# Optimization experiments

Hardware: AMD Instinct MI355X
Metric: run time of the kernel (lower is better)

Reference implementation:

```python
import jax, jax.numpy as jnp
import numpy as np

N = 50000      # nodes
E = 800000     # edges (before self-loops)
IN = 256       # input features
H = 8          # heads
C = 32         # hidden channels per head
OUT = 40       # classes
NEG_SLOPE = 0.2


def setup_inputs() -> dict:
    key = jax.random.key(0)
    ks = jax.random.split(key, 12)
    sd = lambda k, sh: (jax.random.normal(k, sh, jnp.float32) * 0.05)
    return {
        "x": jax.random.normal(ks[0], (N, IN), jnp.float32),
        "edge_index": jax.random.randint(ks[1], (2, E), 0, N),
        "W1": sd(ks[2], (IN, H * C)),
        "a_src1": sd(ks[3], (H, C)),
        "a_dst1": sd(ks[4], (H, C)),
        "b1": jnp.zeros((C,), jnp.float32),
        "W2": sd(ks[5], (C, H * C)),
        "a_src2": sd(ks[6], (H, C)),
        "a_dst2": sd(ks[7], (H, C)),
        "b2": jnp.zeros((C,), jnp.float32),
        "Wo": sd(ks[8], (C, OUT)),
        "bo": jnp.zeros((OUT,), jnp.float32),
    }


def gat_layer(x, src, dst, n, W, a_src, a_dst, b):
    # x: [N, F]; src/dst: [E'] (self-loops included). concat=False -> mean over heads.
    h = (x @ W).reshape(n, H, C)                       # [N, H, C]
    alpha_src = jnp.sum(h * a_src, axis=-1)            # [N, H]
    alpha_dst = jnp.sum(h * a_dst, axis=-1)            # [N, H]
    e = alpha_src[src] + alpha_dst[dst]                # [E', H]
    e = jnp.where(e > 0, e, NEG_SLOPE * e)             # leaky_relu
    # segment softmax over incoming edges of each dst node
    m = jax.ops.segment_max(e, dst, num_segments=n)    # [N, H]
    ex = jnp.exp(e - m[dst])                           # [E', H]
    s = jax.ops.segment_sum(ex, dst, num_segments=n)   # [N, H]
    alpha = ex / s[dst]                                # [E', H]
    msg = alpha[:, :, None] * h[src]                   # [E', H, C]
    out = jax.ops.segment_sum(msg, dst, num_segments=n)  # [N, H, C]
    return out.mean(axis=1) + b                        # [N, C]


def reference(x, edge_index, W1, a_src1, a_dst1, b1, W2, a_src2, a_dst2, b2, Wo, bo):
    n = x.shape[0]
    loops = jnp.arange(n, dtype=edge_index.dtype)
    src = jnp.concatenate([edge_index[0], loops])      # add self-loops (PyG default)
    dst = jnp.concatenate([edge_index[1], loops])
    h = gat_layer(x, src, dst, n, W1, a_src1, a_dst1, b1)
    h = jax.nn.elu(h)                                  # dropout skipped (eval)
    h = gat_layer(h, src, dst, n, W2, a_src2, a_dst2, b2)
    h = jax.nn.elu(h)
    logits = h @ Wo + bo
    return jax.nn.log_softmax(logits, axis=1)
```

## Files before the change

kernel.cpp:

```cpp
#include <hip/hip_runtime.h>
#include <math.h>

#define N_NODES 50000
#define N_PAD   50016
#define N_EDGES 800000
#define E_TOT   (N_EDGES + N_NODES)
#define F_IN    256
#define NHEAD   8
#define CH      32
#define HC      256
#define OUT_C   40
#define NEG_SLOPE 0.2f
#define SCAN_BLOCKS ((N_NODES + 255) / 256)
#define G_WCVT  ((HC * F_IN + 255) / 256)
#define G_WCVT2 ((HC * CH + 255) / 256)
#define NRANGE  8
#define RANGE_SZ (N_NODES / NRANGE)
#define BIN_CHUNK 2048
#define G_BINCH ((E_TOT + BIN_CHUNK - 1) / BIN_CHUNK)

typedef unsigned short u16;
typedef unsigned int   u32;
typedef unsigned char  u8;
typedef __attribute__((ext_vector_type(8))) short bf16x8;
typedef __attribute__((ext_vector_type(4))) float f32x4;
typedef __attribute__((ext_vector_type(2))) float f32x2;

__device__ __forceinline__ u16 f2bf(float f) {
    union { u32 u; float f; } x; x.f = f;
    u32 u = x.u;
    return (u16)((u + 0x7fffu + ((u >> 16) & 1u)) >> 16);
}
__device__ __forceinline__ float bflo(u32 v) {
    union { u32 u; float f; } x; x.u = v << 16; return x.f;
}
__device__ __forceinline__ u8 f2fp8(float f) {
    return (u8)(__builtin_amdgcn_cvt_pk_fp8_f32(f, f, 0, false) & 0xff);
}
__device__ __forceinline__ bf16x8 pack_bf16x8(float4 a, float4 b) {
    bf16x8 r;
    r[0] = (short)f2bf(a.x); r[1] = (short)f2bf(a.y);
    r[2] = (short)f2bf(a.z); r[3] = (short)f2bf(a.w);
    r[4] = (short)f2bf(b.x); r[5] = (short)f2bf(b.y);
    r[6] = (short)f2bf(b.z); r[7] = (short)f2bf(b.w);
    return r;
}


__global__ __launch_bounds__(256) void cvt_kernel(const float* __restrict__ W1,
        u16* __restrict__ Wt, const float* __restrict__ W2, u16* __restrict__ W2t) {
    int b = blockIdx.x;
    if (b < G_WCVT) {
        int t = b * 256 + threadIdx.x;
        int n = t & 255, k = t >> 8;
        Wt[(size_t)n * F_IN + k] = f2bf(W1[(size_t)k * HC + n]);
    } else {
        int t = (b - G_WCVT) * 256 + threadIdx.x;
        if (t >= HC * CH) return;
        int n = t & 255, k = t >> 8;
        W2t[(size_t)n * CH + k] = f2bf(W2[(size_t)k * HC + n]);
    }
}

__global__ __launch_bounds__(256) void gemm1_mfma(const float* __restrict__ x,
        const u16* __restrict__ Wt, u8* __restrict__ ht8) {
    const int row0 = blockIdx.x * 32;
    const int t    = threadIdx.x;
    const int wave = t >> 6;
    const int lane = t & 63;
    const int l16  = lane & 15;
    const int quad = lane >> 4;
    const int nb   = wave * 64;

    f32x4 acc[2][4];
    #pragma unroll
    for (int m = 0; m < 2; ++m)
        #pragma unroll
        for (int n = 0; n < 4; ++n) acc[m][n] = (f32x4){0.f, 0.f, 0.f, 0.f};

    const int ar0 = min(row0 + l16, N_NODES - 1);
    const int ar1 = min(row0 + 16 + l16, N_NODES - 1);
    const float* a0p = x + (size_t)ar0 * F_IN;
    const float* a1p = x + (size_t)ar1 * F_IN;
    const u16*   bp  = Wt + (size_t)(nb + l16) * F_IN;

    #pragma unroll 1
    for (int k0 = 0; k0 < F_IN; k0 += 32) {
        const int ko = k0 + quad * 8;
        float4 a0lo = *(const float4*)(a0p + ko);
        float4 a0hi = *(const float4*)(a0p + ko + 4);
        float4 a1lo = *(const float4*)(a1p + ko);
        float4 a1hi = *(const float4*)(a1p + ko + 4);
        bf16x8 a0 = pack_bf16x8(a0lo, a0hi);
        bf16x8 a1 = pack_bf16x8(a1lo, a1hi);
        bf16x8 b0 = *(const bf16x8*)(bp + 0 * 16 * F_IN + ko);
        bf16x8 b1 = *(const bf16x8*)(bp + 1 * 16 * F_IN + ko);
        bf16x8 b2 = *(const bf16x8*)(bp + 2 * 16 * F_IN + ko);
        bf16x8 b3 = *(const bf16x8*)(bp + 3 * 16 * F_IN + ko);
        acc[0][0] = __builtin_amdgcn_mfma_f32_16x16x32_bf16(a0, b0, acc[0][0], 0, 0, 0);
        acc[0][1] = __builtin_amdgcn_mfma_f32_16x16x32_bf16(a0, b1, acc[0][1], 0, 0, 0);
        acc[0][2] = __builtin_amdgcn_mfma_f32_16x16x32_bf16(a0, b2, acc[0][2], 0, 0, 0);
        acc[0][3] = __builtin_amdgcn_mfma_f32_16x16x32_bf16(a0, b3, acc[0][3], 0, 0, 0);
        acc[1][0] = __builtin_amdgcn_mfma_f32_16x16x32_bf16(a1, b0, acc[1][0], 0, 0, 0);
        acc[1][1] = __builtin_amdgcn_mfma_f32_16x16x32_bf16(a1, b1, acc[1][1], 0, 0, 0);
        acc[1][2] = __builtin_amdgcn_mfma_f32_16x16x32_bf16(a1, b2, acc[1][2], 0, 0, 0);
        acc[1][3] = __builtin_amdgcn_mfma_f32_16x16x32_bf16(a1, b3, acc[1][3], 0, 0, 0);
    }

    #pragma unroll
    for (int m = 0; m < 2; ++m) {
        #pragma unroll
        for (int r = 0; r < 4; ++r) {
            int row = row0 + m * 16 + quad * 4 + r;
            if (row < N_NODES) {
                u8* hr = ht8 + (size_t)row * HC;
                #pragma unroll
                for (int n = 0; n < 4; ++n) {
                    int col = nb + n * 16 + l16;
                    hr[col] = f2fp8(acc[m][n][r]);
                }
            }
        }
    }
}

__global__ __launch_bounds__(256) void gemm2_mfma(const u16* __restrict__ hmb,
        const u16* __restrict__ W2t, u8* __restrict__ ht8) {
    const int row0 = blockIdx.x * 32;
    const int t    = threadIdx.x;
    const int wave = t >> 6;
    const int lane = t & 63;
    const int l16  = lane & 15;
    const int quad = lane >> 4;
    const int nb   = wave * 64;
    const int ko   = quad * 8;

    const u16* a0p = hmb + (size_t)(row0 + l16) * CH;
    const u16* a1p = a0p + 16 * CH;
    const u16* bp  = W2t + (size_t)(nb + l16) * CH;

    bf16x8 a0 = *(const bf16x8*)(a0p + ko);
    bf16x8 a1 = *(const bf16x8*)(a1p + ko);
    bf16x8 b0 = *(const bf16x8*)(bp + 0 * 16 * CH + ko);
    bf16x8 b1 = *(const bf16x8*)(bp + 1 * 16 * CH + ko);
    bf16x8 b2 = *(const bf16x8*)(bp + 2 * 16 * CH + ko);
    bf16x8 b3 = *(const bf16x8*)(bp + 3 * 16 * CH + ko);

    f32x4 z = (f32x4){0.f, 0.f, 0.f, 0.f};
    f32x4 acc[2][4];
    acc[0][0] = __builtin_amdgcn_mfma_f32_16x16x32_bf16(a0, b0, z, 0, 0, 0);
    acc[0][1] = __builtin_amdgcn_mfma_f32_16x16x32_bf16(a0, b1, z, 0, 0, 0);
    acc[0][2] = __builtin_amdgcn_mfma_f32_16x16x32_bf16(a0, b2, z, 0, 0, 0);
    acc[0][3] = __builtin_amdgcn_mfma_f32_16x16x32_bf16(a0, b3, z, 0, 0, 0);
    acc[1][0] = __builtin_amdgcn_mfma_f32_16x16x32_bf16(a1, b0, z, 0, 0, 0);
    acc[1][1] = __builtin_amdgcn_mfma_f32_16x16x32_bf16(a1, b1, z, 0, 0, 0);
    acc[1][2] = __builtin_amdgcn_mfma_f32_16x16x32_bf16(a1, b2, z, 0, 0, 0);
    acc[1][3] = __builtin_amdgcn_mfma_f32_16x16x32_bf16(a1, b3, z, 0, 0, 0);

    #pragma unroll
    for (int m = 0; m < 2; ++m) {
        #pragma unroll
        for (int r = 0; r < 4; ++r) {
            int row = row0 + m * 16 + quad * 4 + r;
            if (row < N_NODES) {
                u8* hr = ht8 + (size_t)row * HC;
                #pragma unroll
                for (int n = 0; n < 4; ++n) {
                    int col = nb + n * 16 + l16;
                    hr[col] = f2fp8(acc[m][n][r]);
                }
            }
        }
    }
}

__global__ __launch_bounds__(256) void alpha_t_kernel(const u8* __restrict__ ht8,
        const float* __restrict__ a_src, const float* __restrict__ a_dst,
        float* __restrict__ asrc, float* __restrict__ adst) {
    __shared__ float sas[HC], sad[HC];
    for (int i = threadIdx.x; i < HC; i += 256) {
        sas[i] = a_src[i];
        sad[i] = a_dst[i];
    }
    __syncthreads();
    int node = blockIdx.x * 256 + threadIdx.x;
    if (node >= N_NODES) return;
    const uint2* hp = (const uint2*)(ht8 + (size_t)node * HC);
    float s1[NHEAD], s2[NHEAD];
    #pragma unroll
    for (int h = 0; h < NHEAD; ++h) {
        float t1 = 0.f, t2 = 0.f;
        #pragma unroll
        for (int i = 0; i < 4; ++i) {
            uint2 v = hp[h * 4 + i];
            f32x2 p01 = __builtin_amdgcn_cvt_pk_f32_fp8(v.x, false);
            f32x2 p23 = __builtin_amdgcn_cvt_pk_f32_fp8(v.x, true);
            f32x2 p45 = __builtin_amdgcn_cvt_pk_f32_fp8(v.y, false);
            f32x2 p67 = __builtin_amdgcn_cvt_pk_f32_fp8(v.y, true);
            const float* s1p = &sas[h * CH + i * 8];
            const float* s2p = &sad[h * CH + i * 8];
            t1 += p01.x * s1p[0] + p01.y * s1p[1] + p23.x * s1p[2] + p23.y * s1p[3]
                + p45.x * s1p[4] + p45.y * s1p[5] + p67.x * s1p[6] + p67.y * s1p[7];
            t2 += p01.x * s2p[0] + p01.y * s2p[1] + p23.x * s2p[2] + p23.y * s2p[3]
                + p45.x * s2p[4] + p45.y * s2p[5] + p67.x * s2p[6] + p67.y * s2p[7];
        }
        s1[h] = t1; s2[h] = t2;
    }
    float4* o1 = (float4*)(asrc + (size_t)node * NHEAD);
    float4* o2 = (float4*)(adst + (size_t)node * NHEAD);
    o1[0] = make_float4(s1[0], s1[1], s1[2], s1[3]);
    o1[1] = make_float4(s1[4], s1[5], s1[6], s1[7]);
    o2[0] = make_float4(s2[0], s2[1], s2[2], s2[3]);
    o2[1] = make_float4(s2[4], s2[5], s2[6], s2[7]);
}

__global__ __launch_bounds__(256) void deg_kernel(const int* __restrict__ ei,
        int* __restrict__ deg) {
    const int r  = blockIdx.x & (NRANGE - 1);
    const int ch = blockIdx.x >> 3;
    const int lo = r * RANGE_SZ, hi = lo + RANGE_SZ;
    int j0 = ch * BIN_CHUNK + threadIdx.x;
    #pragma unroll
    for (int i = 0; i < BIN_CHUNK / 256; ++i) {
        int j = j0 + i * 256;
        if (j < E_TOT) {
            int d = (j < N_EDGES) ? ei[N_EDGES + j] : (j - N_EDGES);
            if (d >= lo && d < hi) atomicAdd(&deg[d], 1);
        }
    }
}

__device__ __forceinline__ int wave_incl_scan(int v, int lane) {
    #pragma unroll
    for (int d = 1; d < 64; d <<= 1) {
        int u = __shfl_up(v, d, 64);
        if (lane >= d) v += u;
    }
    return v;
}

__global__ __launch_bounds__(256) void scan1_kernel(const int* __restrict__ deg,
        int* __restrict__ rowptr, int* __restrict__ partials) {
    const int t    = blockIdx.x * 256 + threadIdx.x;
    const int lane = threadIdx.x & 63;
    const int wid  = threadIdx.x >> 6;
    int v = (t < N_NODES) ? deg[t] : 0;
    int inc = wave_incl_scan(v, lane);
    __shared__ int wtot[4];
    if (lane == 63) wtot[wid] = inc;
    __syncthreads();
    int woff = 0;
    #pragma unroll
    for (int i = 0; i < 4; ++i) woff += (i < wid) ? wtot[i] : 0;
    if (t < N_NODES) rowptr[t] = inc - v + woff;
    if (threadIdx.x == 255) partials[blockIdx.x] = woff + inc;
}

__global__ __launch_bounds__(256) void scan2_kernel(int* __restrict__ partials) {
    const int t    = threadIdx.x;
    const int lane = t & 63;
    const int wid  = t >> 6;
    int v = (t < SCAN_BLOCKS) ? partials[t] : 0;
    int inc = wave_incl_scan(v, lane);
    __shared__ int wtot[4];
    if (lane == 63) wtot[wid] = inc;
    __syncthreads();
    int woff = 0;
    #pragma unroll
    for (int i = 0; i < 4; ++i) woff += (i < wid) ? wtot[i] : 0;
    __syncthreads();
    if (t < SCAN_BLOCKS) partials[t] = inc - v + woff;
}

__global__ __launch_bounds__(256) void scan3_kernel(int* __restrict__ rowptr,
        int* __restrict__ cursor, const int* __restrict__ partials) {
    const int t = blockIdx.x * 256 + threadIdx.x;
    if (t < N_NODES) {
        int v = rowptr[t] + partials[blockIdx.x];
        rowptr[t] = v;
        cursor[t] = v;
    } else if (t == N_NODES) {
        rowptr[N_NODES] = E_TOT;
    }
}

__global__ __launch_bounds__(256) void scatter_kernel(const int* __restrict__ ei,
        int* __restrict__ cursor, u16* __restrict__ csr_src) {
    const int r  = blockIdx.x & (NRANGE - 1);
    const int ch = blockIdx.x >> 3;
    const int lo = r * RANGE_SZ, hi = lo + RANGE_SZ;
    int j0 = ch * BIN_CHUNK + threadIdx.x;
    #pragma unroll
    for (int i = 0; i < BIN_CHUNK / 256; ++i) {
        int j = j0 + i * 256;
        if (j < E_TOT) {
            int d = (j < N_EDGES) ? ei[N_EDGES + j] : (j - N_EDGES);
            if (d >= lo && d < hi) {
                int s = (j < N_EDGES) ? ei[j] : d;
                int pos = atomicAdd(&cursor[d], 1);
                csr_src[pos] = (u16)s;
            }
        }
    }
}

__global__ __launch_bounds__(256) void attn_kernel(const int* __restrict__ rowptr,
        const u16* __restrict__ csr_src, const float* __restrict__ asrc,
        const float* __restrict__ adst, const u8* __restrict__ ht8,
        const float* __restrict__ b, u16* __restrict__ out) {
    const int wid = (blockIdx.x * 256 + threadIdx.x) >> 6;
    if (wid >= N_NODES) return;
    const int dst  = wid;
    const int lane = threadIdx.x & 63;
    const int q    = lane >> 4;
    const int l16  = lane & 15;
    const int h    = l16 >> 1;
    const float ad_own = adst[dst * NHEAD + h];
    const u8* hbase = ht8 + l16 * 16;

    f32x2 acc2[8];
    #pragma unroll
    for (int i = 0; i < 8; ++i) acc2[i] = (f32x2){0.f, 0.f};
    float wsum = 0.f;

    const int p0 = rowptr[dst], p1 = rowptr[dst + 1];
    const int nt = (p1 - p0 + 7) >> 3;

    float asA = -1e30f, asB = -1e30f;
    uint4 hvA = make_uint4(0u, 0u, 0u, 0u), hvB = make_uint4(0u, 0u, 0u, 0u);
    int e = p0 + q;
    if (e < p1) {
        int s = (int)csr_src[e];
        asA = asrc[s * NHEAD + h];
        hvA = *(const uint4*)(hbase + ((size_t)s << 8));
    }
    if (e + 4 < p1) {
        int s = (int)csr_src[e + 4];
        asB = asrc[s * NHEAD + h];
        hvB = *(const uint4*)(hbase + ((size_t)s << 8));
    }

    for (int it = 0; it < nt; ++it) {
        float aA = asA; uint4 hA = hvA;
        float aB = asB; uint4 hB = hvB;
        asA = -1e30f; asB = -1e30f;
        if (e + 8 < p1) {
            int s = (int)csr_src[e + 8];
            asA = asrc[s * NHEAD + h];
            hvA = *(const uint4*)(hbase + ((size_t)s << 8));
        }
        if (e + 12 < p1) {
            int s = (int)csr_src[e + 12];
            asB = asrc[s * NHEAD + h];
            hvB = *(const uint4*)(hbase + ((size_t)s << 8));
        }
        {
            float x = aA + ad_own;
            x = x > 0.f ? x : NEG_SLOPE * x;
            float w = __expf(x);
            wsum += w;
            f32x2 w2; w2.x = w; w2.y = w;
            acc2[0] = __builtin_elementwise_fma(w2, __builtin_amdgcn_cvt_pk_f32_fp8(hA.x, false), acc2[0]);
            acc2[1] = __builtin_elementwise_fma(w2, __builtin_amdgcn_cvt_pk_f32_fp8(hA.x, true ), acc2[1]);
            acc2[2] = __builtin_elementwise_fma(w2, __builtin_amdgcn_cvt_pk_f32_fp8(hA.y, false), acc2[2]);
            acc2[3] = __builtin_elementwise_fma(w2, __builtin_amdgcn_cvt_pk_f32_fp8(hA.y, true ), acc2[3]);
            acc2[4] = __builtin_elementwise_fma(w2, __builtin_amdgcn_cvt_pk_f32_fp8(hA.z, false), acc2[4]);
            acc2[5] = __builtin_elementwise_fma(w2, __builtin_amdgcn_cvt_pk_f32_fp8(hA.z, true ), acc2[5]);
            acc2[6] = __builtin_elementwise_fma(w2, __builtin_amdgcn_cvt_pk_f32_fp8(hA.w, false), acc2[6]);
            acc2[7] = __builtin_elementwise_fma(w2, __builtin_amdgcn_cvt_pk_f32_fp8(hA.w, true ), acc2[7]);
        }
        {
            float x = aB + ad_own;
            x = x > 0.f ? x : NEG_SLOPE * x;
            float w = __expf(x);
            wsum += w;
            f32x2 w2; w2.x = w; w2.y = w;
            acc2[0] = __builtin_elementwise_fma(w2, __builtin_amdgcn_cvt_pk_f32_fp8(hB.x, false), acc2[0]);
            acc2[1] = __builtin_elementwise_fma(w2, __builtin_amdgcn_cvt_pk_f32_fp8(hB.x, true ), acc2[1]);
            acc2[2] = __builtin_elementwise_fma(w2, __builtin_amdgcn_cvt_pk_f32_fp8(hB.y, false), acc2[2]);
            acc2[3] = __builtin_elementwise_fma(w2, __builtin_amdgcn_cvt_pk_f32_fp8(hB.y, true ), acc2[3]);
            acc2[4] = __builtin_elementwise_fma(w2, __builtin_amdgcn_cvt_pk_f32_fp8(hB.z, false), acc2[4]);
            acc2[5] = __builtin_elementwise_fma(w2, __builtin_amdgcn_cvt_pk_f32_fp8(hB.z, true ), acc2[5]);
            acc2[6] = __builtin_elementwise_fma(w2, __builtin_amdgcn_cvt_pk_f32_fp8(hB.w, false), acc2[6]);
            acc2[7] = __builtin_elementwise_fma(w2, __builtin_amdgcn_cvt_pk_f32_fp8(hB.w, true ), acc2[7]);
        }
        e += 8;
    }

    #pragma unroll
    for (int i = 0; i < 8; ++i) {
        acc2[i].x += __shfl_xor(acc2[i].x, 16, 64);
        acc2[i].y += __shfl_xor(acc2[i].y, 16, 64);
        acc2[i].x += __shfl_xor(acc2[i].x, 32, 64);
        acc2[i].y += __shfl_xor(acc2[i].y, 32, 64);
    }
    wsum += __shfl_xor(wsum, 16, 64);
    wsum += __shfl_xor(wsum, 32, 64);

    float winv = 1.0f / wsum;
    f32x2 winv2; winv2.x = winv; winv2.y = winv;
    #pragma unroll
    for (int i = 0; i < 8; ++i) acc2[i] *= winv2;

    #pragma unroll
    for (int i = 0; i < 8; ++i) {
        acc2[i].x += __shfl_xor(acc2[i].x, 2, 64);
        acc2[i].y += __shfl_xor(acc2[i].y, 2, 64);
        acc2[i].x += __shfl_xor(acc2[i].x, 4, 64);
        acc2[i].y += __shfl_xor(acc2[i].y, 4, 64);
        acc2[i].x += __shfl_xor(acc2[i].x, 8, 64);
        acc2[i].y += __shfl_xor(acc2[i].y, 8, 64);
    }

    if (lane < 2) {
        const int c0 = lane * 16;
        const float4* bp4 = (const float4*)(b + c0);
        float4 b0 = bp4[0], b1 = bp4[1], b2 = bp4[2], b3 = bp4[3];
        float bb[16] = {b0.x, b0.y, b0.z, b0.w, b1.x, b1.y, b1.z, b1.w,
                        b2.x, b2.y, b2.z, b2.w, b3.x, b3.y, b3.z, b3.w};
        u32 d[8];
        #pragma unroll
        for (int i = 0; i < 8; ++i) {
            float v0 = acc2[i].x * 0.125f + bb[2 * i];
            float v1 = acc2[i].y * 0.125f + bb[2 * i + 1];
            v0 = v0 > 0.f ? v0 : (__expf(v0) - 1.f);
            v1 = v1 > 0.f ? v1 : (__expf(v1) - 1.f);
            d[i] = (u32)f2bf(v0) | ((u32)f2bf(v1) << 16);
        }
        uint4* op = (uint4*)(out + (size_t)dst * CH + c0);
        op[0] = make_uint4(d[0], d[1], d[2], d[3]);
        op[1] = make_uint4(d[4], d[5], d[6], d[7]);
    }
}

__global__ __launch_bounds__(256) void out_kernel(const u16* __restrict__ hf,
        const float* __restrict__ Wo, const float* __restrict__ bo,
        float* __restrict__ out) {
    const int wave = threadIdx.x >> 6;
    const int lane = threadIdx.x & 63;
    const int n    = blockIdx.x * 4 + wave;
    __shared__ float hs[4][CH];
    if (n < N_NODES && lane < CH) hs[wave][lane] = bflo((u32)hf[n * CH + lane]);
    __syncthreads();
    if (n >= N_NODES) return;
    float logit = -INFINITY;
    if (lane < OUT_C) {
        float a = bo[lane];
        #pragma unroll
        for (int k = 0; k < CH; ++k) a += hs[wave][k] * Wo[k * OUT_C + lane];
        logit = a;
    }
    float m = logit;
    #pragma unroll
    for (int off = 32; off; off >>= 1) m = fmaxf(m, __shfl_xor(m, off, 64));
    float ex = (lane < OUT_C) ? __expf(logit - m) : 0.f;
    float ssum = ex;
    #pragma unroll
    for (int off = 32; off; off >>= 1) ssum += __shfl_xor(ssum, off, 64);
    if (lane < OUT_C) out[(size_t)n * OUT_C + lane] = logit - m - __logf(ssum);
}

extern "C" void kernel_launch(void* const* d_in, const int* in_sizes, int n_in,
                              void* d_out, int out_size, void* d_ws, size_t ws_size,
                              hipStream_t stream) {
    const float* x      = (const float*)d_in[0];
    const int*   ei     = (const int*)  d_in[1];
    const float* W1     = (const float*)d_in[2];
    const float* a_src1 = (const float*)d_in[3];
    const float* a_dst1 = (const float*)d_in[4];
    const float* b1     = (const float*)d_in[5];
    const float* W2     = (const float*)d_in[6];
    const float* a_src2 = (const float*)d_in[7];
    const float* a_dst2 = (const float*)d_in[8];
    const float* b2     = (const float*)d_in[9];
    const float* Wo     = (const float*)d_in[10];
    const float* bo     = (const float*)d_in[11];
    float* out = (float*)d_out;

    char* ws = (char*)d_ws;
    size_t off = 0;
    auto carve = [&](size_t bytes) { char* p = ws + off; off += (bytes + 255) & ~(size_t)255; return p; };
    u8*    ht8     = (u8*)   carve((size_t)N_NODES * HC);
    u16*   Wt      = (u16*)  carve((size_t)HC * F_IN * 2);
    u16*   W2t     = (u16*)  carve((size_t)HC * CH * 2);
    float* asrc    = (float*)carve((size_t)N_NODES * NHEAD * 4);
    float* adst    = (float*)carve((size_t)N_NODES * NHEAD * 4);
    u16*   hmid    = (u16*)  carve((size_t)N_PAD * CH * 2);
    u16*   hout    = (u16*)  carve((size_t)N_NODES * CH * 2);
    int*   deg     = (int*)  carve((size_t)N_NODES * 4);
    int*   rowptr  = (int*)  carve((size_t)(N_NODES + 1) * 4);
    int*   cursor  = (int*)  carve((size_t)N_NODES * 4);
    u16*   csr_src = (u16*)  carve((size_t)E_TOT * 2);
    int*   partials= (int*)  carve((size_t)SCAN_BLOCKS * 4);

    const int g_cvt   = G_WCVT + G_WCVT2;
    const int g_bin   = G_BINCH * NRANGE;
    const int g_gemm  = (N_NODES + 31) / 32;
    const int g_node  = (N_NODES + 255) / 256;
    const int g_attn  = (N_NODES * 64 + 255) / 256;
    const int g_out   = (N_NODES + 3) / 4;

    (void)hipMemsetAsync(deg, 0, (size_t)N_NODES * 4, stream);
    cvt_kernel<<<g_cvt, 256, 0, stream>>>(W1, Wt, W2, W2t);
    deg_kernel<<<g_bin, 256, 0, stream>>>(ei, deg);
    scan1_kernel<<<SCAN_BLOCKS, 256, 0, stream>>>(deg, rowptr, partials);
    scan2_kernel<<<1, 256, 0, stream>>>(partials);
    scan3_kernel<<<SCAN_BLOCKS, 256, 0, stream>>>(rowptr, cursor, partials);
    scatter_kernel<<<g_bin, 256, 0, stream>>>(ei, cursor, csr_src);

    gemm1_mfma<<<g_gemm, 256, 0, stream>>>(x, Wt, ht8);
    alpha_t_kernel<<<g_node, 256, 0, stream>>>(ht8, a_src1, a_dst1, asrc, adst);
    attn_kernel<<<g_attn, 256, 0, stream>>>(rowptr, csr_src, asrc, adst, ht8, b1, hmid);

    gemm2_mfma<<<g_gemm, 256, 0, stream>>>(hmid, W2t, ht8);
    alpha_t_kernel<<<g_node, 256, 0, stream>>>(ht8, a_src2, a_dst2, asrc, adst);
    attn_kernel<<<g_attn, 256, 0, stream>>>(rowptr, csr_src, asrc, adst, ht8, b2, hout);

    out_kernel<<<g_out, 256, 0, stream>>>(hout, Wo, bo, out);
}
```

Before: 387.9 us.

## Fuse alpha into GEMM epilogues, output head into attn, deg into cvt, stage A in LDS

The attention-logit dot products are now computed in the GEMM epilogues from fp32 accumulators with cross-lane shuffles, which removes the separate alpha kernels and their re-read of the fp8 features. The degree count is merged into the weight-conversion launch, and the final linear layer plus log-softmax is folded into the second attention kernel, removing out_kernel and the hout buffer. GEMM1 now stages bf16-converted x in swizzled shared memory, so each row is converted once per block instead of once per wave. The costs are more shuffles and a larger epilogue in the GEMMs, and a serial 16-step shuffle-and-FMA loop for the output head inside each attention wave.

```diff
diff --git a/kernel.cpp b/kernel.cpp
--- a/kernel.cpp
+++ b/kernel.cpp
@@ -18,6 +18,7 @@
 #define RANGE_SZ (N_NODES / NRANGE)
 #define BIN_CHUNK 2048
 #define G_BINCH ((E_TOT + BIN_CHUNK - 1) / BIN_CHUNK)
+#define G_BIN   (G_BINCH * NRANGE)
 
 typedef unsigned short u16;
 typedef unsigned int   u32;
@@ -37,40 +38,118 @@
 __device__ __forceinline__ u8 f2fp8(float f) {
     return (u8)(__builtin_amdgcn_cvt_pk_fp8_f32(f, f, 0, false) & 0xff);
 }
-__device__ __forceinline__ bf16x8 pack_bf16x8(float4 a, float4 b) {
-    bf16x8 r;
-    r[0] = (short)f2bf(a.x); r[1] = (short)f2bf(a.y);
-    r[2] = (short)f2bf(a.z); r[3] = (short)f2bf(a.w);
-    r[4] = (short)f2bf(b.x); r[5] = (short)f2bf(b.y);
-    r[6] = (short)f2bf(b.z); r[7] = (short)f2bf(b.w);
-    return r;
-}
 
 
 __global__ __launch_bounds__(256) void cvt_kernel(const float* __restrict__ W1,
-        u16* __restrict__ Wt, const float* __restrict__ W2, u16* __restrict__ W2t) {
+        u16* __restrict__ Wt, const float* __restrict__ W2, u16* __restrict__ W2t,
+        const int* __restrict__ ei, int* __restrict__ deg) {
     int b = blockIdx.x;
-    if (b < G_WCVT) {
-        int t = b * 256 + threadIdx.x;
+    if (b < G_BIN) {
+        const int r  = b & (NRANGE - 1);
+        const int ch = b >> 3;
+        const int lo = r * RANGE_SZ, hi = lo + RANGE_SZ;
+        int j0 = ch * BIN_CHUNK + threadIdx.x;
+        #pragma unroll
+        for (int i = 0; i < BIN_CHUNK / 256; ++i) {
+            int j = j0 + i * 256;
+            if (j < E_TOT) {
+                int d = (j < N_EDGES) ? ei[N_EDGES + j] : (j - N_EDGES);
+                if (d >= lo && d < hi) atomicAdd(&deg[d], 1);
+            }
+        }
+    } else if (b < G_BIN + G_WCVT) {
+        int t = (b - G_BIN) * 256 + threadIdx.x;
         int n = t & 255, k = t >> 8;
         Wt[(size_t)n * F_IN + k] = f2bf(W1[(size_t)k * HC + n]);
     } else {
-        int t = (b - G_WCVT) * 256 + threadIdx.x;
+        int t = (b - G_BIN - G_WCVT) * 256 + threadIdx.x;
         if (t >= HC * CH) return;
         int n = t & 255, k = t >> 8;
         W2t[(size_t)n * CH + k] = f2bf(W2[(size_t)k * HC + n]);
     }
 }
 
+__device__ __forceinline__ void gemm_epilogue(f32x4 acc[2][4], int row0, int quad,
+        int l16, int nb, const float* __restrict__ a_src,
+        const float* __restrict__ a_dst, u8* __restrict__ ht8,
+        float* __restrict__ asrc, float* __restrict__ adst) {
+    #pragma unroll
+    for (int m = 0; m < 2; ++m) {
+        #pragma unroll
+        for (int r = 0; r < 4; ++r) {
+            int row = row0 + m * 16 + quad * 4 + r;
+            if (row < N_NODES) {
+                u8* hr = ht8 + (size_t)row * HC;
+                #pragma unroll
+                for (int n = 0; n < 4; ++n)
+                    hr[nb + n * 16 + l16] = f2fp8(acc[m][n][r]);
+            }
+        }
+    }
+    const int hA = nb >> 5;
+    const float sA0 = a_src[hA * 32 + l16],       sA1 = a_src[hA * 32 + 16 + l16];
+    const float sB0 = a_src[(hA + 1) * 32 + l16], sB1 = a_src[(hA + 1) * 32 + 16 + l16];
+    const float dA0 = a_dst[hA * 32 + l16],       dA1 = a_dst[hA * 32 + 16 + l16];
+    const float dB0 = a_dst[(hA + 1) * 32 + l16], dB1 = a_dst[(hA + 1) * 32 + 16 + l16];
+    #pragma unroll
+    for (int m = 0; m < 2; ++m) {
+        #pragma unroll
+        for (int r = 0; r < 4; ++r) {
+            float pa = acc[m][0][r] * sA0 + acc[m][1][r] * sA1;
+            float pb = acc[m][2][r] * sB0 + acc[m][3][r] * sB1;
+            float qa = acc[m][0][r] * dA0 + acc[m][1][r] * dA1;
+            float qb = acc[m][2][r] * dB0 + acc[m][3][r] * dB1;
+            #pragma unroll
+            for (int off = 1; off < 16; off <<= 1) {
+                pa += __shfl_xor(pa, off, 64);
+                pb += __shfl_xor(pb, off, 64);
+                qa += __shfl_xor(qa, off, 64);
+                qb += __shfl_xor(qb, off, 64);
+            }
+            int row = row0 + m * 16 + quad * 4 + r;
+            if (l16 == 0 && row < N_NODES) {
+                asrc[row * NHEAD + hA]     = pa;
+                asrc[row * NHEAD + hA + 1] = pb;
+                adst[row * NHEAD + hA]     = qa;
+                adst[row * NHEAD + hA + 1] = qb;
+            }
+        }
+    }
+}
+
 __global__ __launch_bounds__(256) void gemm1_mfma(const float* __restrict__ x,
-        const u16* __restrict__ Wt, u8* __restrict__ ht8) {
+        const u16* __restrict__ Wt, const float* __restrict__ a_src,
+        const float* __restrict__ a_dst, u8* __restrict__ ht8,
+        float* __restrict__ asrc, float* __restrict__ adst) {
+    __shared__ u16 As[32 * 256];
     const int row0 = blockIdx.x * 32;
     const int t    = threadIdx.x;
+
+    {
+        const int r   = t >> 3;
+        const int sub = t & 7;
+        const int gr  = min(row0 + r, N_NODES - 1);
+        const float4* xr = (const float4*)(x + (size_t)gr * F_IN);
+        const int sw = (r & 7) << 4;
+        char* Ar = (char*)As + r * 512;
+        #pragma unroll
+        for (int i = 0; i < 8; ++i) {
+            int f4 = i * 8 + sub;
+            float4 v = xr[f4];
+            u32 lo = (u32)f2bf(v.x) | ((u32)f2bf(v.y) << 16);
+            u32 hi = (u32)f2bf(v.z) | ((u32)f2bf(v.w) << 16);
+            *(uint2*)(Ar + ((f4 * 8) ^ sw)) = make_uint2(lo, hi);
+        }
+    }
+    __syncthreads();
+
     const int wave = t >> 6;
     const int lane = t & 63;
     const int l16  = lane & 15;
     const int quad = lane >> 4;
     const int nb   = wave * 64;
+    const int swr  = (l16 & 7) << 4;
+    const char* Ab = (const char*)As;
 
     f32x4 acc[2][4];
     #pragma unroll
@@ -78,21 +157,13 @@
         #pragma unroll
         for (int n = 0; n < 4; ++n) acc[m][n] = (f32x4){0.f, 0.f, 0.f, 0.f};
 
-    const int ar0 = min(row0 + l16, N_NODES - 1);
-    const int ar1 = min(row0 + 16 + l16, N_NODES - 1);
-    const float* a0p = x + (size_t)ar0 * F_IN;
-    const float* a1p = x + (size_t)ar1 * F_IN;
-    const u16*   bp  = Wt + (size_t)(nb + l16) * F_IN;
+    const u16* bp = Wt + (size_t)(nb + l16) * F_IN;
 
     #pragma unroll 1
     for (int k0 = 0; k0 < F_IN; k0 += 32) {
         const int ko = k0 + quad * 8;
-        float4 a0lo = *(const float4*)(a0p + ko);
-        float4 a0hi = *(const float4*)(a0p + ko + 4);
-        float4 a1lo = *(const float4*)(a1p + ko);
-        float4 a1hi = *(const float4*)(a1p + ko + 4);
-        bf16x8 a0 = pack_bf16x8(a0lo, a0hi);
-        bf16x8 a1 = pack_bf16x8(a1lo, a1hi);
+        bf16x8 a0 = *(const bf16x8*)(Ab + l16 * 512 + ((ko * 2) ^ swr));
+        bf16x8 a1 = *(const bf16x8*)(Ab + (16 + l16) * 512 + ((ko * 2) ^ swr));
         bf16x8 b0 = *(const bf16x8*)(bp + 0 * 16 * F_IN + ko);
         bf16x8 b1 = *(const bf16x8*)(bp + 1 * 16 * F_IN + ko);
         bf16x8 b2 = *(const bf16x8*)(bp + 2 * 16 * F_IN + ko);
@@ -106,26 +177,13 @@
         acc[1][2] = __builtin_amdgcn_mfma_f32_16x16x32_bf16(a1, b2, acc[1][2], 0, 0, 0);
         acc[1][3] = __builtin_amdgcn_mfma_f32_16x16x32_bf16(a1, b3, acc[1][3], 0, 0, 0);
     }
-
-    #pragma unroll
-    for (int m = 0; m < 2; ++m) {
-        #pragma unroll
-        for (int r = 0; r < 4; ++r) {
-            int row = row0 + m * 16 + quad * 4 + r;
-            if (row < N_NODES) {
-                u8* hr = ht8 + (size_t)row * HC;
-                #pragma unroll
-                for (int n = 0; n < 4; ++n) {
-                    int col = nb + n * 16 + l16;
-                    hr[col] = f2fp8(acc[m][n][r]);
-                }
-            }
-        }
-    }
+    gemm_epilogue(acc, row0, quad, l16, nb, a_src, a_dst, ht8, asrc, adst);
 }
 
 __global__ __launch_bounds__(256) void gemm2_mfma(const u16* __restrict__ hmb,
-        const u16* __restrict__ W2t, u8* __restrict__ ht8) {
+        const u16* __restrict__ W2t, const float* __restrict__ a_src,
+        const float* __restrict__ a_dst, u8* __restrict__ ht8,
+        float* __restrict__ asrc, float* __restrict__ adst) {
     const int row0 = blockIdx.x * 32;
     const int t    = threadIdx.x;
     const int wave = t >> 6;
@@ -157,77 +215,7 @@
     acc[1][2] = __builtin_amdgcn_mfma_f32_16x16x32_bf16(a1, b2, z, 0, 0, 0);
     acc[1][3] = __builtin_amdgcn_mfma_f32_16x16x32_bf16(a1, b3, z, 0, 0, 0);
 
-    #pragma unroll
-    for (int m = 0; m < 2; ++m) {
-        #pragma unroll
-        for (int r = 0; r < 4; ++r) {
-            int row = row0 + m * 16 + quad * 4 + r;
-            if (row < N_NODES) {
-                u8* hr = ht8 + (size_t)row * HC;
-                #pragma unroll
-                for (int n = 0; n < 4; ++n) {
-                    int col = nb + n * 16 + l16;
-                    hr[col] = f2fp8(acc[m][n][r]);
-                }
-            }
-        }
-    }
-}
-
-__global__ __launch_bounds__(256) void alpha_t_kernel(const u8* __restrict__ ht8,
-        const float* __restrict__ a_src, const float* __restrict__ a_dst,
-        float* __restrict__ asrc, float* __restrict__ adst) {
-    __shared__ float sas[HC], sad[HC];
-    for (int i = threadIdx.x; i < HC; i += 256) {
-        sas[i] = a_src[i];
-        sad[i] = a_dst[i];
-    }
-    __syncthreads();
-    int node = blockIdx.x * 256 + threadIdx.x;
-    if (node >= N_NODES) return;
-    const uint2* hp = (const uint2*)(ht8 + (size_t)node * HC);
-    float s1[NHEAD], s2[NHEAD];
-    #pragma unroll
-    for (int h = 0; h < NHEAD; ++h) {
-        float t1 = 0.f, t2 = 0.f;
-        #pragma unroll
-        for (int i = 0; i < 4; ++i) {
-            uint2 v = hp[h * 4 + i];
-            f32x2 p01 = __builtin_amdgcn_cvt_pk_f32_fp8(v.x, false);
-            f32x2 p23 = __builtin_amdgcn_cvt_pk_f32_fp8(v.x, true);
-            f32x2 p45 = __builtin_amdgcn_cvt_pk_f32_fp8(v.y, false);
-            f32x2 p67 = __builtin_amdgcn_cvt_pk_f32_fp8(v.y, true);
-            const float* s1p = &sas[h * CH + i * 8];
-            const float* s2p = &sad[h * CH + i * 8];
-            t1 += p01.x * s1p[0] + p01.y * s1p[1] + p23.x * s1p[2] + p23.y * s1p[3]
-                + p45.x * s1p[4] + p45.y * s1p[5] + p67.x * s1p[6] + p67.y * s1p[7];
-            t2 += p01.x * s2p[0] + p01.y * s2p[1] + p23.x * s2p[2] + p23.y * s2p[3]
-                + p45.x * s2p[4] + p45.y * s2p[5] + p67.x * s2p[6] + p67.y * s2p[7];
-        }
-        s1[h] = t1; s2[h] = t2;
-    }
-    float4* o1 = (float4*)(asrc + (size_t)node * NHEAD);
-    float4* o2 = (float4*)(adst + (size_t)node * NHEAD);
-    o1[0] = make_float4(s1[0], s1[1], s1[2], s1[3]);
-    o1[1] = make_float4(s1[4], s1[5], s1[6], s1[7]);
-    o2[0] = make_float4(s2[0], s2[1], s2[2], s2[3]);
-    o2[1] = make_float4(s2[4], s2[5], s2[6], s2[7]);
-}
-
-__global__ __launch_bounds__(256) void deg_kernel(const int* __restrict__ ei,
-        int* __restrict__ deg) {
-    const int r  = blockIdx.x & (NRANGE - 1);
-    const int ch = blockIdx.x >> 3;
-    const int lo = r * RANGE_SZ, hi = lo + RANGE_SZ;
-    int j0 = ch * BIN_CHUNK + threadIdx.x;
-    #pragma unroll
-    for (int i = 0; i < BIN_CHUNK / 256; ++i) {
-        int j = j0 + i * 256;
-        if (j < E_TOT) {
-            int d = (j < N_EDGES) ? ei[N_EDGES + j] : (j - N_EDGES);
-            if (d >= lo && d < hi) atomicAdd(&deg[d], 1);
-        }
-    }
+    gemm_epilogue(acc, row0, quad, l16, nb, a_src, a_dst, ht8, asrc, adst);
 }
 
 __device__ __forceinline__ int wave_incl_scan(int v, int lane) {
@@ -304,10 +292,13 @@
     }
 }
 
+template<bool FINAL>
 __global__ __launch_bounds__(256) void attn_kernel(const int* __restrict__ rowptr,
         const u16* __restrict__ csr_src, const float* __restrict__ asrc,
         const float* __restrict__ adst, const u8* __restrict__ ht8,
-        const float* __restrict__ b, u16* __restrict__ out) {
+        const float* __restrict__ b, u16* __restrict__ out_mid,
+        const float* __restrict__ Wo, const float* __restrict__ bo,
+        float* __restrict__ out_final) {
     const int wid = (blockIdx.x * 256 + threadIdx.x) >> 6;
     if (wid >= N_NODES) return;
     const int dst  = wid;
@@ -412,52 +403,59 @@
         acc2[i].y += __shfl_xor(acc2[i].y, 8, 64);
     }
 
-    if (lane < 2) {
-        const int c0 = lane * 16;
-        const float4* bp4 = (const float4*)(b + c0);
+    if constexpr (!FINAL) {
+        if (lane < 2) {
+            const int c0 = lane * 16;
+            const float4* bp4 = (const float4*)(b + c0);
+            float4 b0 = bp4[0], b1 = bp4[1], b2 = bp4[2], b3 = bp4[3];
+            float bb[16] = {b0.x, b0.y, b0.z, b0.w, b1.x, b1.y, b1.z, b1.w,
+                            b2.x, b2.y, b2.z, b2.w, b3.x, b3.y, b3.z, b3.w};
+            u32 d[8];
+            #pragma unroll
+            for (int i = 0; i < 8; ++i) {
+                float v0 = acc2[i].x * 0.125f + bb[2 * i];
+                float v1 = acc2[i].y * 0.125f + bb[2 * i + 1];
+                v0 = v0 > 0.f ? v0 : (__expf(v0) - 1.f);
+                v1 = v1 > 0.f ? v1 : (__expf(v1) - 1.f);
+                d[i] = (u32)f2bf(v0) | ((u32)f2bf(v1) << 16);
+            }
+            uint4* op = (uint4*)(out_mid + (size_t)dst * CH + c0);
+            op[0] = make_uint4(d[0], d[1], d[2], d[3]);
+            op[1] = make_uint4(d[4], d[5], d[6], d[7]);
+        }
+    } else {
+        const int c0f = (lane & 1) * 16;
+        const float4* bp4 = (const float4*)(b + c0f);
         float4 b0 = bp4[0], b1 = bp4[1], b2 = bp4[2], b3 = bp4[3];
         float bb[16] = {b0.x, b0.y, b0.z, b0.w, b1.x, b1.y, b1.z, b1.w,
                         b2.x, b2.y, b2.z, b2.w, b3.x, b3.y, b3.z, b3.w};
-        u32 d[8];
+        float v[16];
         #pragma unroll
         for (int i = 0; i < 8; ++i) {
             float v0 = acc2[i].x * 0.125f + bb[2 * i];
             float v1 = acc2[i].y * 0.125f + bb[2 * i + 1];
-            v0 = v0 > 0.f ? v0 : (__expf(v0) - 1.f);
-            v1 = v1 > 0.f ? v1 : (__expf(v1) - 1.f);
-            d[i] = (u32)f2bf(v0) | ((u32)f2bf(v1) << 16);
-        }
-        uint4* op = (uint4*)(out + (size_t)dst * CH + c0);
-        op[0] = make_uint4(d[0], d[1], d[2], d[3]);
-        op[1] = make_uint4(d[4], d[5], d[6], d[7]);
-    }
-}
-
-__global__ __launch_bounds__(256) void out_kernel(const u16* __restrict__ hf,
-        const float* __restrict__ Wo, const float* __restrict__ bo,
-        float* __restrict__ out) {
-    const int wave = threadIdx.x >> 6;
-    const int lane = threadIdx.x & 63;
-    const int n    = blockIdx.x * 4 + wave;
-    __shared__ float hs[4][CH];
-    if (n < N_NODES && lane < CH) hs[wave][lane] = bflo((u32)hf[n * CH + lane]);
-    __syncthreads();
-    if (n >= N_NODES) return;
-    float logit = -INFINITY;
-    if (lane < OUT_C) {
-        float a = bo[lane];
-        #pragma unroll
-        for (int k = 0; k < CH; ++k) a += hs[wave][k] * Wo[k * OUT_C + lane];
-        logit = a;
-    }
-    float m = logit;
-    #pragma unroll
-    for (int off = 32; off; off >>= 1) m = fmaxf(m, __shfl_xor(m, off, 64));
-    float ex = (lane < OUT_C) ? __expf(logit - m) : 0.f;
-    float ssum = ex;
-    #pragma unroll
-    for (int off = 32; off; off >>= 1) ssum += __shfl_xor(ssum, off, 64);
-    if (lane < OUT_C) out[(size_t)n * OUT_C + lane] = logit - m - __logf(ssum);
+            v[2 * i]     = v0 > 0.f ? v0 : (__expf(v0) - 1.f);
+            v[2 * i + 1] = v1 > 0.f ? v1 : (__expf(v1) - 1.f);
+        }
+        float logit = -INFINITY;
+        if (lane < OUT_C) logit = bo[lane];
+        #pragma unroll
+        for (int k = 0; k < 16; ++k) {
+            float h0 = __shfl(v[k], 0, 64);
+            float h1 = __shfl(v[k], 1, 64);
+            if (lane < OUT_C)
+                logit += h0 * Wo[k * OUT_C + lane] + h1 * Wo[(16 + k) * OUT_C + lane];
+        }
+        float mx = logit;
+        #pragma unroll
+        for (int off = 32; off; off >>= 1) mx = fmaxf(mx, __shfl_xor(mx, off, 64));
+        float ex = (lane < OUT_C) ? __expf(logit - mx) : 0.f;
+        float ss = ex;
+        #pragma unroll
+        for (int off = 32; off; off >>= 1) ss += __shfl_xor(ss, off, 64);
+        if (lane < OUT_C)
+            out_final[(size_t)dst * OUT_C + lane] = logit - mx - __logf(ss);
+    }
 }
 
 extern "C" void kernel_launch(void* const* d_in, const int* in_sizes, int n_in,
@@ -486,35 +484,28 @@
     float* asrc    = (float*)carve((size_t)N_NODES * NHEAD * 4);
     float* adst    = (float*)carve((size_t)N_NODES * NHEAD * 4);
     u16*   hmid    = (u16*)  carve((size_t)N_PAD * CH * 2);
-    u16*   hout    = (u16*)  carve((size_t)N_NODES * CH * 2);
     int*   deg     = (int*)  carve((size_t)N_NODES * 4);
     int*   rowptr  = (int*)  carve((size_t)(N_NODES + 1) * 4);
     int*   cursor  = (int*)  carve((size_t)N_NODES * 4);
     u16*   csr_src = (u16*)  carve((size_t)E_TOT * 2);
     int*   partials= (int*)  carve((size_t)SCAN_BLOCKS * 4);
 
-    const int g_cvt   = G_WCVT + G_WCVT2;
-    const int g_bin   = G_BINCH * NRANGE;
+    const int g_cvt   = G_BIN + G_WCVT + G_WCVT2;
     const int g_gemm  = (N_NODES + 31) / 32;
-    const int g_node  = (N_NODES + 255) / 256;
     const int g_attn  = (N_NODES * 64 + 255) / 256;
-    const int g_out   = (N_NODES + 3) / 4;
 
     (void)hipMemsetAsync(deg, 0, (size_t)N_NODES * 4, stream);
-    cvt_kernel<<<g_cvt, 256, 0, stream>>>(W1, Wt, W2, W2t);
-    deg_kernel<<<g_bin, 256, 0, stream>>>(ei, deg);
+    cvt_kernel<<<g_cvt, 256, 0, stream>>>(W1, Wt, W2, W2t, ei, deg);
     scan1_kernel<<<SCAN_BLOCKS, 256, 0, stream>>>(deg, rowptr, partials);
     scan2_kernel<<<1, 256, 0, stream>>>(partials);
     scan3_kernel<<<SCAN_BLOCKS, 256, 0, stream>>>(rowptr, cursor, partials);
-    scatter_kernel<<<g_bin, 256, 0, stream>>>(ei, cursor, csr_src);
-
-    gemm1_mfma<<<g_gemm, 256, 0, stream>>>(x, Wt, ht8);
-    alpha_t_kernel<<<g_node, 256, 0, stream>>>(ht8, a_src1, a_dst1, asrc, adst);
-    attn_kernel<<<g_attn, 256, 0, stream>>>(rowptr, csr_src, asrc, adst, ht8, b1, hmid);
-
-    gemm2_mfma<<<g_gemm, 256, 0, stream>>>(hmid, W2t, ht8);
-    alpha_t_kernel<<<g_node, 256, 0, stream>>>(ht8, a_src2, a_dst2, asrc, adst);
-    attn_kernel<<<g_attn, 256, 0, stream>>>(rowptr, csr_src, asrc, adst, ht8, b2, hout);
-
-    out_kernel<<<g_out, 256, 0, stream>>>(hout, Wo, bo, out);
-}
+    scatter_kernel<<<G_BIN, 256, 0, stream>>>(ei, cursor, csr_src);
+
+    gemm1_mfma<<<g_gemm, 256, 0, stream>>>(x, Wt, a_src1, a_dst1, ht8, asrc, adst);
+    attn_kernel<false><<<g_attn, 256, 0, stream>>>(rowptr, csr_src, asrc, adst,
+                                                   ht8, b1, hmid, nullptr, nullptr, nullptr);
+
+    gemm2_mfma<<<g_gemm, 256, 0, stream>>>(hmid, W2t, a_src2, a_dst2, ht8, asrc, adst);
+    attn_kernel<true><<<g_attn, 256, 0, stream>>>(rowptr, csr_src, asrc, adst,
+                                                  ht8, b2, nullptr, Wo, bo, out);
+}
```

New measurement: 380.7 us. About the same (-1.9%).
